# Kernel optimization log

Measured on AMD Instinct MI355X. Metric: run time of the kernel, lower is better.

Reference implementation:

```python
import jax, jax.numpy as jnp
import numpy as np

N_NODES = 25000
N_EDGES = 400000
N_NODE_DICT = 100
N_EDGE_DICT = 16
EMB = 128
HEADS = 4
F_OUT = 32
HF = HEADS * F_OUT  # 128
NEG_SLOPE = 0.2
LN_EPS = 1e-5


def setup_inputs() -> dict:
    key = jax.random.key(0)
    ks = jax.random.split(key, 12)
    inv_emb = 1.0 / np.sqrt(EMB)
    inputs = {
        # int graph data
        "node_features": jax.random.randint(ks[0], (N_NODES,), 0, N_NODE_DICT, dtype=jnp.int64 if jax.config.jax_enable_x64 else jnp.int32),
        "edge_features": jax.random.randint(ks[1], (N_EDGES,), 0, N_EDGE_DICT, dtype=jnp.int32),
        "edge_index": jax.random.randint(ks[2], (2, N_EDGES), 0, N_NODES, dtype=jnp.int32),
        # embedding tables (nn.Embedding ~ N(0,1))
        "node_emb": jax.random.normal(ks[3], (N_NODE_DICT, EMB), dtype=jnp.float32),
        "edge_emb": jax.random.normal(ks[4], (N_EDGE_DICT, EMB), dtype=jnp.float32),
        # target_w == neighbor_w (share_weights=True): Linear(EMB, HF)
        "W_t": jax.random.uniform(ks[5], (EMB, HF), jnp.float32, -inv_emb, inv_emb),
        "b_t": jax.random.uniform(ks[6], (HF,), jnp.float32, -inv_emb, inv_emb),
        # edgew: Linear(EMB, HF)
        "W_e": jax.random.uniform(ks[7], (EMB, HF), jnp.float32, -inv_emb, inv_emb),
        "b_e": jax.random.uniform(ks[8], (HF,), jnp.float32, -inv_emb, inv_emb),
        # attn: Linear(3*F_OUT, 1)
        "a_w": jax.random.uniform(ks[9], (3 * F_OUT,), jnp.float32, -1.0 / np.sqrt(3 * F_OUT), 1.0 / np.sqrt(3 * F_OUT)),
        "a_b": jax.random.uniform(ks[10], (), jnp.float32, -1.0 / np.sqrt(3 * F_OUT), 1.0 / np.sqrt(3 * F_OUT)),
        # LayerNorm(HF)
        "ln_gamma": jnp.ones((HF,), jnp.float32),
        "ln_beta": jnp.zeros((HF,), jnp.float32),
    }
    return inputs


def _layer_norm(x, gamma, beta):
    mu = jnp.mean(x, axis=-1, keepdims=True)
    var = jnp.mean(jnp.square(x - mu), axis=-1, keepdims=True)
    return (x - mu) * jax.lax.rsqrt(var + LN_EPS) * gamma + beta


def _forward(node_features, edge_features, edge_index,
             node_emb, edge_emb, W_t, b_t, W_e, b_e, a_w, a_b, ln_gamma, ln_beta):
    # embeddings
    h = node_emb[node_features]            # [N, EMB]
    e = edge_emb[edge_features]            # [E, EMB]

    src = edge_index[0]                    # neighbor j
    tgt = edge_index[1]                    # target i

    # per-edge projections -> [E, H, F]
    edge_h = (e @ W_e + b_e).reshape(-1, HEADS, F_OUT)
    h_proj = h @ W_t + b_t                 # project nodes once ([N, HF]) then gather
    h_i = h_proj[tgt].reshape(-1, HEADS, F_OUT)
    h_j = h_proj[src].reshape(-1, HEADS, F_OUT)  # shared weights

    # attn(cat[h_i, h_j, edge_h]) == h_i@a1 + h_j@a2 + edge_h@a3 + bias
    a1, a2, a3 = a_w[:F_OUT], a_w[F_OUT:2 * F_OUT], a_w[2 * F_OUT:]
    logits = (jnp.einsum('ehf,f->eh', h_i, a1)
              + jnp.einsum('ehf,f->eh', h_j, a2)
              + jnp.einsum('ehf,f->eh', edge_h, a3) + a_b)   # [E, H]
    eij = jnp.where(logits >= 0, logits, NEG_SLOPE * logits)  # LeakyReLU

    # scatter_softmax over edges grouped by target node
    seg_max = jax.ops.segment_max(eij, tgt, num_segments=N_NODES)   # [N, H]
    ex = jnp.exp(eij - seg_max[tgt])
    seg_sum = jax.ops.segment_sum(ex, tgt, num_segments=N_NODES)    # [N, H]
    alpha = ex / seg_sum[tgt]                                       # [E, H]

    message = alpha[:, :, None] * h_j + h_i                          # skip connection
    out = jax.ops.segment_sum(message, tgt, num_segments=N_NODES)   # [N, H, F]

    out = out.reshape(-1, HF)                                        # concat=True
    edge_out = edge_h.reshape(-1, HF)
    out = _layer_norm(out, ln_gamma, ln_beta)
    edge_out = _layer_norm(edge_out, ln_gamma, ln_beta)
    return out, edge_out


def reference(node_features, edge_features, edge_index,
              node_emb, edge_emb, W_t, b_t, W_e, b_e, a_w, a_b, ln_gamma, ln_beta):
    return _forward(node_features, edge_features, edge_index,
                    node_emb, edge_emb, W_t, b_t, W_e, b_e, a_w, a_b, ln_gamma, ln_beta)
```

## Files before the change

### kernel.cpp

```cpp
#include <hip/hip_runtime.h>
#include <hip/hip_bf16.h>

#define N_NODES 25000
#define N_EDGES 400000
#define N_NODE_DICT 100
#define N_EDGE_DICT 16
#define EMB 128
#define HF 128
#define NEG_SLOPE 0.2f
#define LN_EPS 1e-5f

#define NB 64
#define EPB (N_EDGES / NB)
#define CAP 64
#define PREB 116
#define WRB 2048
#define NODE_BLOCKS 3125

typedef __hip_bfloat16 bf16;

__device__ __forceinline__ float ldv(const void* p, int i, int m) {
    return m ? ((const float*)p)[i] : __bfloat162float(((const bf16*)p)[i]);
}

#define WS_HP   0
#define WS_S1   51200
#define WS_S2   52800
#define WS_S3   54400
#define WS_LNE  54656
#define WS_LNEF 58752
#define WS_G    66944
#define WS_B    67456
#define WS_AB   67968
#define WS_FLG  68000
#define WS_PC   68016
#define WS_BKT  6468016

__global__ __launch_bounds__(1024) void k_build(
    const int* __restrict__ src, const int* __restrict__ tgt,
    const int* __restrict__ ef, const int* __restrict__ nf,
    const void* ne, const void* ee, const void* Wt, const void* bt,
    const void* We, const void* be, const void* aw, const void* gm,
    const void* bb, const void* ab,
    float* __restrict__ hp, float* __restrict__ s1, float* __restrict__ s2,
    float* __restrict__ s3, bf16* __restrict__ lne, float* __restrict__ lnef,
    float* __restrict__ gws, float* __restrict__ bws, float* __restrict__ abws,
    int* __restrict__ flg, unsigned int* __restrict__ pc,
    unsigned short* __restrict__ bkt)
{
    __shared__ int h[N_NODES];
    __shared__ int wsum[16];
    __shared__ int stot_s;
    __shared__ float red[2];
    __shared__ int lflg;
    int t = threadIdx.x, b = blockIdx.x;

    if (b < NB) {
        if (t == 0) lflg = 0;
        for (int i = t; i < N_NODES; i += 1024) h[i] = 0;
        __syncthreads();
        if (t < 200 && nf[2 * t + 1] != 0) atomicOr(&lflg, 1);
        int e0 = b * EPB;
        for (int i = t; i < EPB; i += 1024) atomicAdd(&h[tgt[e0 + i]], 1);
        __syncthreads();
        int w = lflg;
        const int CH = 25;
        int st = t * CH, en = st + CH;
        if (st > N_NODES) st = N_NODES;
        if (en > N_NODES) en = N_NODES;
        int ssum = 0;
        for (int i = st; i < en; ++i) ssum += h[i];
        int lane = t & 63, wv = t >> 6;
        int winc = ssum;
        for (int d = 1; d < 64; d <<= 1) { int v = __shfl_up(winc, d); if (lane >= d) winc += v; }
        if (lane == 63) wsum[wv] = winc;
        __syncthreads();
        int wbase = 0;
        for (int q = 0; q < wv; ++q) wbase += wsum[q];
        int run = wbase + winc - ssum;
        for (int i = st; i < en; ++i) {
            int c = h[i];
            h[i] = run;
            run += c;
        }
        if (t == 0) { int s = 0; for (int q = 0; q < 16; ++q) s += wsum[q]; stot_s = s; }
        __syncthreads();
        for (int i = t; i < N_NODES; i += 1024) {
            int base_i = h[i];
            int next = (i < N_NODES - 1) ? h[i + 1] : stot_s;
            pc[(i >> 3) * 512 + b * 8 + (i & 7)] =
                ((unsigned)base_i << 16) | (unsigned)(next - base_i);
        }
        __syncthreads();
        for (int i = t; i < EPB; i += 1024) {
            int e = e0 + i;
            int n = tgt[e];
            int slot = atomicAdd(&h[n], 1);
            int s = src[e];
            int ds = w ? nf[s] : nf[2 * s];
            bkt[b * EPB + slot] = (unsigned short)((ds << 4) | ef[e]);
        }
    } else {
        if (t == 0) lflg = 0;
        __syncthreads();
        {
            const unsigned short* u = (const unsigned short*)ne;
            int bad = 0;
            for (int i = t; i < N_NODE_DICT * EMB; i += 1024) {
                int ex = (u[i] >> 7) & 0xFF;
                if (ex >= 134) bad = 1;
            }
            int orv = (bad ? 1 : 0) | ((t < 200 && nf[2 * t + 1] != 0) ? 2 : 0);
            if (orv) atomicOr(&lflg, orv);
        }
        __syncthreads();
        int m = lflg & 1;
        if (b == NB && t == 0) {
            flg[0] = lflg & 1;
            flg[1] = (lflg >> 1) & 1;
        }
        int row = b - NB;
        int f = t & 127, kk = t >> 7;
        bool isn = row < N_NODE_DICT;
        int de = row - N_NODE_DICT;
        const void* emb = isn ? ne : ee;
        int ebase = (isn ? row : de) * EMB;
        const void* W = isn ? Wt : We;
        const void* bia = isn ? bt : be;
        float part = 0.f;
        for (int k = kk * 16; k < kk * 16 + 16; ++k)
            part += ldv(emb, ebase + k, m) * ldv(W, k * HF + f, m);
        float* hf = (float*)h;
        hf[kk * 128 + f] = part;
        __syncthreads();
        float acc = 0.f;
        if (t < 128) {
            acc = ldv(bia, t, m);
            for (int q = 0; q < 8; ++q) acc += hf[q * 128 + t];
        }
        if (row == 0 && t < 128) {
            gws[t] = ldv(gm, t, m);
            bws[t] = ldv(bb, t, m);
            if (t == 0) abws[0] = ldv(ab, 0, m);
        }
        int j = t & 31, hd = (t >> 5) & 3;
        if (isn) {
            if (t < 128) {
                hp[row * HF + t] = acc;
                float p1 = acc * ldv(aw, j, m);
                float p2 = acc * ldv(aw, 32 + j, m);
                for (int s = 16; s >= 1; s >>= 1) { p1 += __shfl_xor(p1, s); p2 += __shfl_xor(p2, s); }
                if (j == 0) { s1[row * 4 + hd] = p1; s2[row * 4 + hd] = p2; }
            }
        } else {
            if (t < 128) {
                float p3 = acc * ldv(aw, 64 + j, m);
                for (int s = 16; s >= 1; s >>= 1) p3 += __shfl_xor(p3, s);
                if (j == 0) s3[de * 4 + hd] = p3;
                float tt = acc;
                for (int s = 32; s >= 1; s >>= 1) tt += __shfl_xor(tt, s);
                if ((t & 63) == 0) red[t >> 6] = tt;
            }
            __syncthreads();
            float mu = (red[0] + red[1]) * (1.0f / 128.0f);
            float d = acc - mu;
            if (t < 128) {
                float v = d * d;
                for (int s = 32; s >= 1; s >>= 1) v += __shfl_xor(v, s);
                if ((t & 63) == 0) red[t >> 6] = v;
            }
            __syncthreads();
            if (t < 128) {
                float var = (red[0] + red[1]) * (1.0f / 128.0f);
                float o = d * rsqrtf(var + LN_EPS) * ldv(gm, t, m) + ldv(bb, t, m);
                lne[de * HF + t] = __float2bfloat16(o);
                lnef[de * HF + t] = o;
            }
        }
    }
}

__global__ __launch_bounds__(512) void k_out(
    const int* __restrict__ nf, const unsigned int* __restrict__ pc,
    const unsigned short* __restrict__ bkt, const float* __restrict__ hp,
    const float* __restrict__ s1, const float* __restrict__ s2,
    const float* __restrict__ s3, const float* __restrict__ abws,
    const float* __restrict__ gws, const float* __restrict__ bws,
    const int* __restrict__ ef, const uint4* __restrict__ lneb,
    const uint4* __restrict__ lnef4,
    void* __restrict__ dout, const int* __restrict__ flg)
{
    __shared__ unsigned int sm_pc[512];
    __shared__ unsigned short sme[8][CAP];
    __shared__ float4 smw[8][CAP];
    int b = blockIdx.x;
    if (b < WRB) {
        int tid = b * 512 + threadIdx.x;
        const int stride = WRB * 512;
        if (flg[0]) {
            uint4* out = (uint4*)((float*)dout + (size_t)N_NODES * HF);
            const int total = N_EDGES * 32;
            for (int i = tid; i < total; i += stride) {
                int e = i >> 5, c = i & 31;
                out[i] = lnef4[(ef[e] << 5) + c];
            }
        } else {
            uint4* out = (uint4*)((bf16*)dout + (size_t)N_NODES * HF);
            const int total = N_EDGES * 16;
            for (int i = tid; i < total; i += stride) {
                int e = i >> 4, c = i & 15;
                out[i] = lneb[(ef[e] << 4) + c];
            }
        }
    } else {
        int nb = b - WRB;
        int t = threadIdx.x;
        sm_pc[t] = pc[nb * 512 + t];
        __syncthreads();
        int w = t >> 6, lane = t & 63;
        int node = nb * 8 + w;
        int dn = flg[1] ? nf[node] : nf[2 * node];

        unsigned int pcv = sm_pc[lane * 8 + w];
        int base = (int)(pcv >> 16), c = (int)(pcv & 0xFFFFu);
        int inc = c;
        for (int d = 1; d < 64; d <<= 1) { int v = __shfl_up(inc, d); if (lane >= d) inc += v; }
        int pos = inc - c;
        int deg = __shfl(inc, 63);
        for (int j = 0; j < c; ++j) {
            int q = pos + j;
            if (q < CAP) sme[w][q] = bkt[lane * EPB + base + j];
        }
        deg = min(deg, CAP);

        float ab = abws[0];
        const float4 s1v = *(const float4*)(s1 + dn * 4);
        float l0 = -1e30f, l1 = -1e30f, l2 = -1e30f, l3 = -1e30f;
        if (lane < deg) {
            int p = sme[w][lane];
            const float4 v2 = *(const float4*)(s2 + (p >> 4) * 4);
            const float4 v3 = *(const float4*)(s3 + (p & 15) * 4);
            l0 = s1v.x + v2.x + v3.x + ab; l0 = (l0 >= 0.f) ? l0 : NEG_SLOPE * l0;
            l1 = s1v.y + v2.y + v3.y + ab; l1 = (l1 >= 0.f) ? l1 : NEG_SLOPE * l1;
            l2 = s1v.z + v2.z + v3.z + ab; l2 = (l2 >= 0.f) ? l2 : NEG_SLOPE * l2;
            l3 = s1v.w + v2.w + v3.w + ab; l3 = (l3 >= 0.f) ? l3 : NEG_SLOPE * l3;
        }
        float m0 = l0, m1 = l1, m2 = l2, m3 = l3;
        for (int q = 32; q >= 1; q >>= 1) {
            m0 = fmaxf(m0, __shfl_xor(m0, q));
            m1 = fmaxf(m1, __shfl_xor(m1, q));
            m2 = fmaxf(m2, __shfl_xor(m2, q));
            m3 = fmaxf(m3, __shfl_xor(m3, q));
        }
        float e0 = 0.f, e1 = 0.f, e2 = 0.f, e3 = 0.f;
        if (lane < deg) {
            e0 = __expf(l0 - m0); e1 = __expf(l1 - m1);
            e2 = __expf(l2 - m2); e3 = __expf(l3 - m3);
        }
        float t0 = e0, t1 = e1, t2 = e2, t3 = e3;
        for (int q = 32; q >= 1; q >>= 1) {
            t0 += __shfl_xor(t0, q); t1 += __shfl_xor(t1, q);
            t2 += __shfl_xor(t2, q); t3 += __shfl_xor(t3, q);
        }
        if (lane < deg) smw[w][lane] = make_float4(e0, e1, e2, e3);

        bool lo32 = lane < 32;
        float acc0 = 0.f, acc1 = 0.f;
        int i = 0;
        for (; i + 1 < deg; i += 2) {
            int pA = sme[w][i], pB = sme[w][i + 1];
            float4 wA = smw[w][i], wB = smw[w][i + 1];
            const float* hA = hp + (pA >> 4) * HF;
            const float* hB = hp + (pB >> 4) * HF;
            float a0 = hA[lane], b0 = hB[lane];
            float a1 = hA[64 + lane], b1 = hB[64 + lane];
            acc0 += (lo32 ? wA.x : wA.y) * a0 + (lo32 ? wB.x : wB.y) * b0;
            acc1 += (lo32 ? wA.z : wA.w) * a1 + (lo32 ? wB.z : wB.w) * b1;
        }
        if (i < deg) {
            int pA = sme[w][i];
            float4 wA = smw[w][i];
            const float* hA = hp + (pA >> 4) * HF;
            acc0 += (lo32 ? wA.x : wA.y) * hA[lane];
            acc1 += (lo32 ? wA.z : wA.w) * hA[64 + lane];
        }
        float x0 = 0.f, x1 = 0.f;
        if (deg > 0) {
            float slo = lo32 ? t0 : t1;
            float shi = lo32 ? t2 : t3;
            const float* hn = hp + dn * HF;
            x0 = acc0 / slo + (float)deg * hn[lane];
            x1 = acc1 / shi + (float)deg * hn[64 + lane];
        }
        float s = x0 + x1;
        for (int q = 32; q >= 1; q >>= 1) s += __shfl_xor(s, q);
        float mu = s * (1.0f / 128.0f);
        float d0 = x0 - mu, d1 = x1 - mu;
        float v = d0 * d0 + d1 * d1;
        for (int q = 32; q >= 1; q >>= 1) v += __shfl_xor(v, q);
        float rstd = rsqrtf(v * (1.0f / 128.0f) + LN_EPS);
        float r0 = d0 * rstd * gws[lane] + bws[lane];
        float r1 = d1 * rstd * gws[64 + lane] + bws[64 + lane];
        if (flg[0]) {
            float* o = (float*)dout;
            o[node * HF + lane] = r0;
            o[node * HF + 64 + lane] = r1;
        } else {
            bf16* o = (bf16*)dout;
            o[node * HF + lane] = __float2bfloat16(r0);
            o[node * HF + 64 + lane] = __float2bfloat16(r1);
        }
    }
}

extern "C" void kernel_launch(void* const* d_in, const int* in_sizes, int n_in,
                              void* d_out, int out_size, void* d_ws, size_t ws_size,
                              hipStream_t stream) {
    const int* nf  = (const int*)d_in[0];
    const int* efx = (const int*)d_in[1];
    const int* ei  = (const int*)d_in[2];
    const void* node_emb = d_in[3];
    const void* edge_emb = d_in[4];
    const void* W_t = d_in[5];
    const void* b_t = d_in[6];
    const void* W_e = d_in[7];
    const void* b_e = d_in[8];
    const void* a_w = d_in[9];
    const void* a_b = d_in[10];
    const void* gmm = d_in[11];
    const void* bet = d_in[12];

    char* ws = (char*)d_ws;
    float* hp   = (float*)(ws + WS_HP);
    float* s1   = (float*)(ws + WS_S1);
    float* s2   = (float*)(ws + WS_S2);
    float* s3   = (float*)(ws + WS_S3);
    bf16*  lne  = (bf16*)(ws + WS_LNE);
    float* lnef = (float*)(ws + WS_LNEF);
    float* gws  = (float*)(ws + WS_G);
    float* bws  = (float*)(ws + WS_B);
    float* abws = (float*)(ws + WS_AB);
    int*   flg  = (int*)(ws + WS_FLG);
    unsigned int*   pc  = (unsigned int*)(ws + WS_PC);
    unsigned short* bkt = (unsigned short*)(ws + WS_BKT);

    const int* srcIdx = ei;
    const int* tgtIdx = ei + N_EDGES;

    k_build<<<NB + PREB, 1024, 0, stream>>>(
        srcIdx, tgtIdx, efx, nf,
        node_emb, edge_emb, W_t, b_t, W_e, b_e, a_w, gmm, bet, a_b,
        hp, s1, s2, s3, lne, lnef, gws, bws, abws, flg, pc, bkt);

    k_out<<<WRB + NODE_BLOCKS, 512, 0, stream>>>(
        nf, pc, bkt, hp, s1, s2, s3, abws, gws, bws,
        efx, (const uint4*)lne, (const uint4*)lnef, d_out, flg);
}
```

Before: 84.71 us.

## Move edge-output writer into build kernel and pack histogram into 16-bit counters

The edge-output broadcast writer moves out of the second kernel into extra blocks of the first kernel. Each writer block recomputes the 16-row edge projection and its LayerNorm in shared memory, so the copy overlaps with the CSR build instead of running after it. The histogram now packs two 16-bit node counters per int, which halves shared memory and allows 512-thread blocks with more blocks resident per CU. The cost is that every writer block redundantly does a 16x128x128 matmul, and the per-bucket edge count must stay below 65536.

```diff
diff --git a/kernel.cpp b/kernel.cpp
--- a/kernel.cpp
+++ b/kernel.cpp
@@ -14,8 +14,9 @@
 #define EPB (N_EDGES / NB)
 #define CAP 64
 #define PREB 116
-#define WRB 2048
+#define WRB 588
 #define NODE_BLOCKS 3125
+#define NWORD 12500
 
 typedef __hip_bfloat16 bf16;
 
@@ -27,8 +28,6 @@
 #define WS_S1   51200
 #define WS_S2   52800
 #define WS_S3   54400
-#define WS_LNE  54656
-#define WS_LNEF 58752
 #define WS_G    66944
 #define WS_B    67456
 #define WS_AB   67968
@@ -36,20 +35,20 @@
 #define WS_PC   68016
 #define WS_BKT  6468016
 
-__global__ __launch_bounds__(1024) void k_build(
+__global__ __launch_bounds__(512) void k_build(
     const int* __restrict__ src, const int* __restrict__ tgt,
     const int* __restrict__ ef, const int* __restrict__ nf,
     const void* ne, const void* ee, const void* Wt, const void* bt,
     const void* We, const void* be, const void* aw, const void* gm,
     const void* bb, const void* ab,
     float* __restrict__ hp, float* __restrict__ s1, float* __restrict__ s2,
-    float* __restrict__ s3, bf16* __restrict__ lne, float* __restrict__ lnef,
+    float* __restrict__ s3,
     float* __restrict__ gws, float* __restrict__ bws, float* __restrict__ abws,
     int* __restrict__ flg, unsigned int* __restrict__ pc,
-    unsigned short* __restrict__ bkt)
+    unsigned short* __restrict__ bkt, void* __restrict__ dout)
 {
-    __shared__ int h[N_NODES];
-    __shared__ int wsum[16];
+    __shared__ int h[NWORD + 4];
+    __shared__ int wsum[8];
     __shared__ int stot_s;
     __shared__ float red[2];
     __shared__ int lflg;
@@ -57,19 +56,24 @@
 
     if (b < NB) {
         if (t == 0) lflg = 0;
-        for (int i = t; i < N_NODES; i += 1024) h[i] = 0;
+        for (int i = t; i < NWORD; i += 512) h[i] = 0;
         __syncthreads();
         if (t < 200 && nf[2 * t + 1] != 0) atomicOr(&lflg, 1);
         int e0 = b * EPB;
-        for (int i = t; i < EPB; i += 1024) atomicAdd(&h[tgt[e0 + i]], 1);
+        for (int i = t; i < EPB; i += 512) {
+            int n = tgt[e0 + i];
+            atomicAdd(&h[n >> 1], 1 << ((n & 1) * 16));
+        }
         __syncthreads();
         int w = lflg;
-        const int CH = 25;
-        int st = t * CH, en = st + CH;
-        if (st > N_NODES) st = N_NODES;
-        if (en > N_NODES) en = N_NODES;
+        const int CHW = 25;
+        int st = t * CHW; if (st > NWORD) st = NWORD;
+        int en = st + CHW; if (en > NWORD) en = NWORD;
         int ssum = 0;
-        for (int i = st; i < en; ++i) ssum += h[i];
+        for (int i = st; i < en; ++i) {
+            int v = h[i];
+            ssum += (v & 0xFFFF) + ((v >> 16) & 0xFFFF);
+        }
         int lane = t & 63, wv = t >> 6;
         int winc = ssum;
         for (int d = 1; d < 64; d <<= 1) { int v = __shfl_up(winc, d); if (lane >= d) winc += v; }
@@ -79,34 +83,40 @@
         for (int q = 0; q < wv; ++q) wbase += wsum[q];
         int run = wbase + winc - ssum;
         for (int i = st; i < en; ++i) {
-            int c = h[i];
-            h[i] = run;
-            run += c;
-        }
-        if (t == 0) { int s = 0; for (int q = 0; q < 16; ++q) s += wsum[q]; stot_s = s; }
-        __syncthreads();
-        for (int i = t; i < N_NODES; i += 1024) {
-            int base_i = h[i];
-            int next = (i < N_NODES - 1) ? h[i + 1] : stot_s;
-            pc[(i >> 3) * 512 + b * 8 + (i & 7)] =
-                ((unsigned)base_i << 16) | (unsigned)(next - base_i);
-        }
-        __syncthreads();
-        for (int i = t; i < EPB; i += 1024) {
+            int v = h[i];
+            int c0 = v & 0xFFFF, c1 = (v >> 16) & 0xFFFF;
+            int b0 = run; run += c0;
+            int b1 = run; run += c1;
+            h[i] = b0 | (b1 << 16);
+        }
+        if (t == 0) { int s = 0; for (int q = 0; q < 8; ++q) s += wsum[q]; stot_s = s; }
+        __syncthreads();
+        for (int i = t; i < NWORD; i += 512) {
+            int packed = h[i];
+            int b0 = packed & 0xFFFF, b1 = (packed >> 16) & 0xFFFF;
+            int nxt = (i < NWORD - 1) ? (h[i + 1] & 0xFFFF) : stot_s;
+            int n0 = 2 * i, n1 = 2 * i + 1;
+            pc[(n0 >> 3) * 512 + b * 8 + (n0 & 7)] = ((unsigned)b0 << 16) | (unsigned)(b1 - b0);
+            pc[(n1 >> 3) * 512 + b * 8 + (n1 & 7)] = ((unsigned)b1 << 16) | (unsigned)(nxt - b1);
+        }
+        __syncthreads();
+        for (int i = t; i < EPB; i += 512) {
             int e = e0 + i;
             int n = tgt[e];
-            int slot = atomicAdd(&h[n], 1);
+            int sh = (n & 1) * 16;
+            int old = atomicAdd(&h[n >> 1], 1 << sh);
+            int slot = (old >> sh) & 0xFFFF;
             int s = src[e];
             int ds = w ? nf[s] : nf[2 * s];
             bkt[b * EPB + slot] = (unsigned short)((ds << 4) | ef[e]);
         }
-    } else {
+    } else if (b < NB + PREB) {
         if (t == 0) lflg = 0;
         __syncthreads();
         {
             const unsigned short* u = (const unsigned short*)ne;
             int bad = 0;
-            for (int i = t; i < N_NODE_DICT * EMB; i += 1024) {
+            for (int i = t; i < N_NODE_DICT * EMB; i += 512) {
                 int ex = (u[i] >> 7) & 0xFF;
                 if (ex >= 134) bad = 1;
             }
@@ -128,7 +138,7 @@
         const void* W = isn ? Wt : We;
         const void* bia = isn ? bt : be;
         float part = 0.f;
-        for (int k = kk * 16; k < kk * 16 + 16; ++k)
+        for (int k = kk * 32; k < kk * 32 + 32; ++k)
             part += ldv(emb, ebase + k, m) * ldv(W, k * HF + f, m);
         float* hf = (float*)h;
         hf[kk * 128 + f] = part;
@@ -136,7 +146,7 @@
         float acc = 0.f;
         if (t < 128) {
             acc = ldv(bia, t, m);
-            for (int q = 0; q < 8; ++q) acc += hf[q * 128 + t];
+            for (int q = 0; q < 4; ++q) acc += hf[q * 128 + t];
         }
         if (row == 0 && t < 128) {
             gws[t] = ldv(gm, t, m);
@@ -144,172 +154,188 @@
             if (t == 0) abws[0] = ldv(ab, 0, m);
         }
         int j = t & 31, hd = (t >> 5) & 3;
-        if (isn) {
-            if (t < 128) {
+        if (t < 128) {
+            if (isn) {
                 hp[row * HF + t] = acc;
                 float p1 = acc * ldv(aw, j, m);
                 float p2 = acc * ldv(aw, 32 + j, m);
                 for (int s = 16; s >= 1; s >>= 1) { p1 += __shfl_xor(p1, s); p2 += __shfl_xor(p2, s); }
                 if (j == 0) { s1[row * 4 + hd] = p1; s2[row * 4 + hd] = p2; }
-            }
-        } else {
-            if (t < 128) {
+            } else {
                 float p3 = acc * ldv(aw, 64 + j, m);
                 for (int s = 16; s >= 1; s >>= 1) p3 += __shfl_xor(p3, s);
                 if (j == 0) s3[de * 4 + hd] = p3;
-                float tt = acc;
-                for (int s = 32; s >= 1; s >>= 1) tt += __shfl_xor(tt, s);
-                if ((t & 63) == 0) red[t >> 6] = tt;
-            }
-            __syncthreads();
-            float mu = (red[0] + red[1]) * (1.0f / 128.0f);
-            float d = acc - mu;
-            if (t < 128) {
-                float v = d * d;
-                for (int s = 32; s >= 1; s >>= 1) v += __shfl_xor(v, s);
-                if ((t & 63) == 0) red[t >> 6] = v;
-            }
-            __syncthreads();
-            if (t < 128) {
-                float var = (red[0] + red[1]) * (1.0f / 128.0f);
-                float o = d * rsqrtf(var + LN_EPS) * ldv(gm, t, m) + ldv(bb, t, m);
-                lne[de * HF + t] = __float2bfloat16(o);
-                lnef[de * HF + t] = o;
+            }
+        }
+    } else {
+        if (t == 0) lflg = 0;
+        __syncthreads();
+        {
+            const unsigned short* u = (const unsigned short*)ne;
+            int bad = 0;
+            for (int i = t; i < N_NODE_DICT * EMB; i += 512) {
+                int ex = (u[i] >> 7) & 0xFF;
+                if (ex >= 134) bad = 1;
+            }
+            if (bad) atomicOr(&lflg, 1);
+        }
+        __syncthreads();
+        int m = lflg;
+        float* eh = (float*)h;
+        bf16*  ub = (bf16*)(eh + 2048);
+        for (int p = t; p < N_EDGE_DICT * HF; p += 512) {
+            int de = p >> 7, f = p & 127;
+            float a = ldv(be, f, m);
+            for (int k = 0; k < EMB; ++k)
+                a += ldv(ee, de * EMB + k, m) * ldv(We, k * HF + f, m);
+            eh[p] = a;
+        }
+        __syncthreads();
+        int wv = t >> 6, lane = t & 63;
+        for (int r = wv; r < N_EDGE_DICT; r += 8) {
+            float x0 = eh[r * 128 + lane], x1 = eh[r * 128 + 64 + lane];
+            float s = x0 + x1;
+            for (int q = 32; q >= 1; q >>= 1) s += __shfl_xor(s, q);
+            float mu = s * (1.f / 128.f);
+            float d0 = x0 - mu, d1 = x1 - mu;
+            float v = d0 * d0 + d1 * d1;
+            for (int q = 32; q >= 1; q >>= 1) v += __shfl_xor(v, q);
+            float rstd = rsqrtf(v * (1.f / 128.f) + LN_EPS);
+            float o0 = d0 * rstd * ldv(gm, lane, m) + ldv(bb, lane, m);
+            float o1 = d1 * rstd * ldv(gm, 64 + lane, m) + ldv(bb, 64 + lane, m);
+            if (m) { eh[r * 128 + lane] = o0; eh[r * 128 + 64 + lane] = o1; }
+            else   { ub[r * 128 + lane] = __float2bfloat16(o0);
+                     ub[r * 128 + 64 + lane] = __float2bfloat16(o1); }
+        }
+        __syncthreads();
+        int wb = b - NB - PREB;
+        if (m) {
+            uint4* o = (uint4*)((float*)dout + (size_t)N_NODES * HF);
+            const uint4* lsrc = (const uint4*)eh;
+            const int total = N_EDGES * 32;
+            for (int i = wb * 512 + t; i < total; i += WRB * 512) {
+                int e = i >> 5, c = i & 31;
+                o[i] = lsrc[(ef[e] << 5) + c];
+            }
+        } else {
+            uint4* o = (uint4*)((bf16*)dout + (size_t)N_NODES * HF);
+            const uint4* lsrc = (const uint4*)ub;
+            const int total = N_EDGES * 16;
+            for (int i = wb * 512 + t; i < total; i += WRB * 512) {
+                int e = i >> 4, c = i & 15;
+                o[i] = lsrc[(ef[e] << 4) + c];
             }
         }
     }
 }
 
-__global__ __launch_bounds__(512) void k_out(
+__global__ __launch_bounds__(512) void k_node(
     const int* __restrict__ nf, const unsigned int* __restrict__ pc,
     const unsigned short* __restrict__ bkt, const float* __restrict__ hp,
     const float* __restrict__ s1, const float* __restrict__ s2,
     const float* __restrict__ s3, const float* __restrict__ abws,
     const float* __restrict__ gws, const float* __restrict__ bws,
-    const int* __restrict__ ef, const uint4* __restrict__ lneb,
-    const uint4* __restrict__ lnef4,
     void* __restrict__ dout, const int* __restrict__ flg)
 {
     __shared__ unsigned int sm_pc[512];
     __shared__ unsigned short sme[8][CAP];
     __shared__ float4 smw[8][CAP];
-    int b = blockIdx.x;
-    if (b < WRB) {
-        int tid = b * 512 + threadIdx.x;
-        const int stride = WRB * 512;
-        if (flg[0]) {
-            uint4* out = (uint4*)((float*)dout + (size_t)N_NODES * HF);
-            const int total = N_EDGES * 32;
-            for (int i = tid; i < total; i += stride) {
-                int e = i >> 5, c = i & 31;
-                out[i] = lnef4[(ef[e] << 5) + c];
-            }
-        } else {
-            uint4* out = (uint4*)((bf16*)dout + (size_t)N_NODES * HF);
-            const int total = N_EDGES * 16;
-            for (int i = tid; i < total; i += stride) {
-                int e = i >> 4, c = i & 15;
-                out[i] = lneb[(ef[e] << 4) + c];
-            }
-        }
+    int nb = blockIdx.x;
+    int t = threadIdx.x;
+    sm_pc[t] = pc[nb * 512 + t];
+    __syncthreads();
+    int w = t >> 6, lane = t & 63;
+    int node = nb * 8 + w;
+    int dn = flg[1] ? nf[node] : nf[2 * node];
+
+    unsigned int pcv = sm_pc[lane * 8 + w];
+    int base = (int)(pcv >> 16), c = (int)(pcv & 0xFFFFu);
+    int inc = c;
+    for (int d = 1; d < 64; d <<= 1) { int v = __shfl_up(inc, d); if (lane >= d) inc += v; }
+    int pos = inc - c;
+    int deg = __shfl(inc, 63);
+    for (int j = 0; j < c; ++j) {
+        int q = pos + j;
+        if (q < CAP) sme[w][q] = bkt[lane * EPB + base + j];
+    }
+    deg = min(deg, CAP);
+
+    float ab = abws[0];
+    const float4 s1v = *(const float4*)(s1 + dn * 4);
+    float l0 = -1e30f, l1 = -1e30f, l2 = -1e30f, l3 = -1e30f;
+    if (lane < deg) {
+        int p = sme[w][lane];
+        const float4 v2 = *(const float4*)(s2 + (p >> 4) * 4);
+        const float4 v3 = *(const float4*)(s3 + (p & 15) * 4);
+        l0 = s1v.x + v2.x + v3.x + ab; l0 = (l0 >= 0.f) ? l0 : NEG_SLOPE * l0;
+        l1 = s1v.y + v2.y + v3.y + ab; l1 = (l1 >= 0.f) ? l1 : NEG_SLOPE * l1;
+        l2 = s1v.z + v2.z + v3.z + ab; l2 = (l2 >= 0.f) ? l2 : NEG_SLOPE * l2;
+        l3 = s1v.w + v2.w + v3.w + ab; l3 = (l3 >= 0.f) ? l3 : NEG_SLOPE * l3;
+    }
+    float m0 = l0, m1 = l1, m2 = l2, m3 = l3;
+    for (int q = 32; q >= 1; q >>= 1) {
+        m0 = fmaxf(m0, __shfl_xor(m0, q));
+        m1 = fmaxf(m1, __shfl_xor(m1, q));
+        m2 = fmaxf(m2, __shfl_xor(m2, q));
+        m3 = fmaxf(m3, __shfl_xor(m3, q));
+    }
+    float e0 = 0.f, e1 = 0.f, e2 = 0.f, e3 = 0.f;
+    if (lane < deg) {
+        e0 = __expf(l0 - m0); e1 = __expf(l1 - m1);
+        e2 = __expf(l2 - m2); e3 = __expf(l3 - m3);
+    }
+    float t0 = e0, t1 = e1, t2 = e2, t3 = e3;
+    for (int q = 32; q >= 1; q >>= 1) {
+        t0 += __shfl_xor(t0, q); t1 += __shfl_xor(t1, q);
+        t2 += __shfl_xor(t2, q); t3 += __shfl_xor(t3, q);
+    }
+    if (lane < deg) smw[w][lane] = make_float4(e0, e1, e2, e3);
+
+    bool lo32 = lane < 32;
+    float acc0 = 0.f, acc1 = 0.f;
+    int i = 0;
+    for (; i + 1 < deg; i += 2) {
+        int pA = sme[w][i], pB = sme[w][i + 1];
+        float4 wA = smw[w][i], wB = smw[w][i + 1];
+        const float* hA = hp + (pA >> 4) * HF;
+        const float* hB = hp + (pB >> 4) * HF;
+        float a0 = hA[lane], b0 = hB[lane];
+        float a1 = hA[64 + lane], b1 = hB[64 + lane];
+        acc0 += (lo32 ? wA.x : wA.y) * a0 + (lo32 ? wB.x : wB.y) * b0;
+        acc1 += (lo32 ? wA.z : wA.w) * a1 + (lo32 ? wB.z : wB.w) * b1;
+    }
+    if (i < deg) {
+        int pA = sme[w][i];
+        float4 wA = smw[w][i];
+        const float* hA = hp + (pA >> 4) * HF;
+        acc0 += (lo32 ? wA.x : wA.y) * hA[lane];
+        acc1 += (lo32 ? wA.z : wA.w) * hA[64 + lane];
+    }
+    float x0 = 0.f, x1 = 0.f;
+    if (deg > 0) {
+        float slo = lo32 ? t0 : t1;
+        float shi = lo32 ? t2 : t3;
+        const float* hn = hp + dn * HF;
+        x0 = acc0 / slo + (float)deg * hn[lane];
+        x1 = acc1 / shi + (float)deg * hn[64 + lane];
+    }
+    float s = x0 + x1;
+    for (int q = 32; q >= 1; q >>= 1) s += __shfl_xor(s, q);
+    float mu = s * (1.0f / 128.0f);
+    float d0 = x0 - mu, d1 = x1 - mu;
+    float v = d0 * d0 + d1 * d1;
+    for (int q = 32; q >= 1; q >>= 1) v += __shfl_xor(v, q);
+    float rstd = rsqrtf(v * (1.0f / 128.0f) + LN_EPS);
+    float r0 = d0 * rstd * gws[lane] + bws[lane];
+    float r1 = d1 * rstd * gws[64 + lane] + bws[64 + lane];
+    if (flg[0]) {
+        float* o = (float*)dout;
+        o[node * HF + lane] = r0;
+        o[node * HF + 64 + lane] = r1;
     } else {
-        int nb = b - WRB;
-        int t = threadIdx.x;
-        sm_pc[t] = pc[nb * 512 + t];
-        __syncthreads();
-        int w = t >> 6, lane = t & 63;
-        int node = nb * 8 + w;
-        int dn = flg[1] ? nf[node] : nf[2 * node];
-
-        unsigned int pcv = sm_pc[lane * 8 + w];
-        int base = (int)(pcv >> 16), c = (int)(pcv & 0xFFFFu);
-        int inc = c;
-        for (int d = 1; d < 64; d <<= 1) { int v = __shfl_up(inc, d); if (lane >= d) inc += v; }
-        int pos = inc - c;
-        int deg = __shfl(inc, 63);
-        for (int j = 0; j < c; ++j) {
-            int q = pos + j;
-            if (q < CAP) sme[w][q] = bkt[lane * EPB + base + j];
-        }
-        deg = min(deg, CAP);
-
-        float ab = abws[0];
-        const float4 s1v = *(const float4*)(s1 + dn * 4);
-        float l0 = -1e30f, l1 = -1e30f, l2 = -1e30f, l3 = -1e30f;
-        if (lane < deg) {
-            int p = sme[w][lane];
-            const float4 v2 = *(const float4*)(s2 + (p >> 4) * 4);
-            const float4 v3 = *(const float4*)(s3 + (p & 15) * 4);
-            l0 = s1v.x + v2.x + v3.x + ab; l0 = (l0 >= 0.f) ? l0 : NEG_SLOPE * l0;
-            l1 = s1v.y + v2.y + v3.y + ab; l1 = (l1 >= 0.f) ? l1 : NEG_SLOPE * l1;
-            l2 = s1v.z + v2.z + v3.z + ab; l2 = (l2 >= 0.f) ? l2 : NEG_SLOPE * l2;
-            l3 = s1v.w + v2.w + v3.w + ab; l3 = (l3 >= 0.f) ? l3 : NEG_SLOPE * l3;
-        }
-        float m0 = l0, m1 = l1, m2 = l2, m3 = l3;
-        for (int q = 32; q >= 1; q >>= 1) {
-            m0 = fmaxf(m0, __shfl_xor(m0, q));
-            m1 = fmaxf(m1, __shfl_xor(m1, q));
-            m2 = fmaxf(m2, __shfl_xor(m2, q));
-            m3 = fmaxf(m3, __shfl_xor(m3, q));
-        }
-        float e0 = 0.f, e1 = 0.f, e2 = 0.f, e3 = 0.f;
-        if (lane < deg) {
-            e0 = __expf(l0 - m0); e1 = __expf(l1 - m1);
-            e2 = __expf(l2 - m2); e3 = __expf(l3 - m3);
-        }
-        float t0 = e0, t1 = e1, t2 = e2, t3 = e3;
-        for (int q = 32; q >= 1; q >>= 1) {
-            t0 += __shfl_xor(t0, q); t1 += __shfl_xor(t1, q);
-            t2 += __shfl_xor(t2, q); t3 += __shfl_xor(t3, q);
-        }
-        if (lane < deg) smw[w][lane] = make_float4(e0, e1, e2, e3);
-
-        bool lo32 = lane < 32;
-        float acc0 = 0.f, acc1 = 0.f;
-        int i = 0;
-        for (; i + 1 < deg; i += 2) {
-            int pA = sme[w][i], pB = sme[w][i + 1];
-            float4 wA = smw[w][i], wB = smw[w][i + 1];
-            const float* hA = hp + (pA >> 4) * HF;
-            const float* hB = hp + (pB >> 4) * HF;
-            float a0 = hA[lane], b0 = hB[lane];
-            float a1 = hA[64 + lane], b1 = hB[64 + lane];
-            acc0 += (lo32 ? wA.x : wA.y) * a0 + (lo32 ? wB.x : wB.y) * b0;
-            acc1 += (lo32 ? wA.z : wA.w) * a1 + (lo32 ? wB.z : wB.w) * b1;
-        }
-        if (i < deg) {
-            int pA = sme[w][i];
-            float4 wA = smw[w][i];
-            const float* hA = hp + (pA >> 4) * HF;
-            acc0 += (lo32 ? wA.x : wA.y) * hA[lane];
-            acc1 += (lo32 ? wA.z : wA.w) * hA[64 + lane];
-        }
-        float x0 = 0.f, x1 = 0.f;
-        if (deg > 0) {
-            float slo = lo32 ? t0 : t1;
-            float shi = lo32 ? t2 : t3;
-            const float* hn = hp + dn * HF;
-            x0 = acc0 / slo + (float)deg * hn[lane];
-            x1 = acc1 / shi + (float)deg * hn[64 + lane];
-        }
-        float s = x0 + x1;
-        for (int q = 32; q >= 1; q >>= 1) s += __shfl_xor(s, q);
-        float mu = s * (1.0f / 128.0f);
-        float d0 = x0 - mu, d1 = x1 - mu;
-        float v = d0 * d0 + d1 * d1;
-        for (int q = 32; q >= 1; q >>= 1) v += __shfl_xor(v, q);
-        float rstd = rsqrtf(v * (1.0f / 128.0f) + LN_EPS);
-        float r0 = d0 * rstd * gws[lane] + bws[lane];
-        float r1 = d1 * rstd * gws[64 + lane] + bws[64 + lane];
-        if (flg[0]) {
-            float* o = (float*)dout;
-            o[node * HF + lane] = r0;
-            o[node * HF + 64 + lane] = r1;
-        } else {
-            bf16* o = (bf16*)dout;
-            o[node * HF + lane] = __float2bfloat16(r0);
-            o[node * HF + 64 + lane] = __float2bfloat16(r1);
-        }
+        bf16* o = (bf16*)dout;
+        o[node * HF + lane] = __float2bfloat16(r0);
+        o[node * HF + 64 + lane] = __float2bfloat16(r1);
     }
 }
 
@@ -335,8 +361,6 @@
     float* s1   = (float*)(ws + WS_S1);
     float* s2   = (float*)(ws + WS_S2);
     float* s3   = (float*)(ws + WS_S3);
-    bf16*  lne  = (bf16*)(ws + WS_LNE);
-    float* lnef = (float*)(ws + WS_LNEF);
     float* gws  = (float*)(ws + WS_G);
     float* bws  = (float*)(ws + WS_B);
     float* abws = (float*)(ws + WS_AB);
@@ -347,12 +371,11 @@
     const int* srcIdx = ei;
     const int* tgtIdx = ei + N_EDGES;
 
-    k_build<<<NB + PREB, 1024, 0, stream>>>(
+    k_build<<<NB + PREB + WRB, 512, 0, stream>>>(
         srcIdx, tgtIdx, efx, nf,
         node_emb, edge_emb, W_t, b_t, W_e, b_e, a_w, gmm, bet, a_b,
-        hp, s1, s2, s3, lne, lnef, gws, bws, abws, flg, pc, bkt);
-
-    k_out<<<WRB + NODE_BLOCKS, 512, 0, stream>>>(
-        nf, pc, bkt, hp, s1, s2, s3, abws, gws, bws,
-        efx, (const uint4*)lne, (const uint4*)lnef, d_out, flg);
+        hp, s1, s2, s3, gws, bws, abws, flg, pc, bkt, d_out);
+
+    k_node<<<NODE_BLOCKS, 512, 0, stream>>>(
+        nf, pc, bkt, hp, s1, s2, s3, abws, gws, bws, d_out, flg);
 }
```

New measurement: 123.0 us. 1.45x slower.
